# Kernel optimization log

Hardware: AMD Instinct MI355X
Metric: run time of the kernel (lower is better)

Reference implementation:

```python
import math
import jax, jax.numpy as jnp
import numpy as np

MAX_LEN = 2048
D_HEAD = 64
B, H, S = 4, 16, 1024


def setup_inputs() -> dict:
    key = jax.random.key(0)
    kq, kk, kp = jax.random.split(key, 3)
    q = jax.random.normal(kq, (B, H, S, D_HEAD), dtype=jnp.float32)
    k = jax.random.normal(kk, (B, H, S, D_HEAD), dtype=jnp.float32)
    pos_table = jax.random.normal(kp, (MAX_LEN, D_HEAD), dtype=jnp.float32)
    return {"q": q, "k": k, "pos_table": pos_table}


def reference(q, k, pos_table):
    d_head = q.shape[-1]
    seq_len = q.shape[2]
    max_len = pos_table.shape[0]
    scale = 1.0 / math.sqrt(d_head)
    # attention gates: (b,h,s,s)
    gates = jax.nn.sigmoid(jnp.einsum('bhsd,bhtd->bhst', q, k) * scale)
    # context positions: weighted sum of key indices -> (b,h,s)
    positions = jnp.arange(seq_len, dtype=q.dtype)
    ctx_pos = jnp.einsum('bhst,t->bhs', gates, positions)
    ctx_pos = jnp.clip(ctx_pos, 0.0, float(max_len - 2))
    pos_floor = ctx_pos.astype(jnp.int32)  # (b,h,s)
    pos_frac = (ctx_pos - pos_floor.astype(q.dtype))[..., None]  # (b,h,s,1)
    emb_floor = pos_table[pos_floor]  # (b,h,s,d)
    emb_ceil = pos_table[jnp.minimum(pos_floor + 1, max_len - 1)]
    pos_emb = emb_floor + pos_frac * (emb_ceil - emb_floor)  # (b,h,s,d)
    # bias: (b,h,s,s)
    bias = jnp.einsum('bhsd,bhtd->bhst', q, pos_emb)
    return bias
```

## Files before the change

### kernel.cpp

```cpp
#include <hip/hip_runtime.h>

#define Bb_ 4
#define Hh_ 16
#define Ss_ 1024
#define DH 64
#define MAXLEN 2048
#define BH (Bb_*Hh_)
#define LDST 72

typedef __attribute__((ext_vector_type(8))) short short8;
typedef __attribute__((ext_vector_type(4))) float floatx4;
typedef __attribute__((ext_vector_type(4))) unsigned short ushort4v;

static __device__ __forceinline__ unsigned short f2bf(float f) {
    unsigned int u = __builtin_bit_cast(unsigned int, f);
    u = (u + 0x7fffu + ((u >> 16) & 1u)) >> 16;
    return (unsigned short)u;
}

static __device__ __forceinline__ void stage_tile(unsigned short* lds,
                                                  const float* __restrict__ g,
                                                  int tid) {
#pragma unroll
    for (int it = 0; it < 8; ++it) {
        int idx = it * 1024 + tid * 4;
        int row = idx >> 6, col = idx & 63;
        const float4 v = *reinterpret_cast<const float4*>(g + row * 64 + col);
        ushort4v o = { f2bf(v.x), f2bf(v.y), f2bf(v.z), f2bf(v.w) };
        *reinterpret_cast<ushort4v*>(lds + row * LDST + col) = o;
    }
}

__global__ __launch_bounds__(256, 2)
void ctx_kernel(const float* __restrict__ q, const float* __restrict__ k,
                float* __restrict__ ctx) {
    __shared__ __align__(16) unsigned short Ab[128 * LDST];
    __shared__ __align__(16) unsigned short Kb[128 * LDST];

    int bx = blockIdx.x;
    int bh = bx >> 3, mt = bx & 7;
    int m0 = mt << 7;
    int tid = threadIdx.x;
    int lane = tid & 63, w = tid >> 6;
    int lo = lane & 15, quad = lane >> 4;

    stage_tile(Ab, q + (size_t)(bh * Ss_ + m0) * DH, tid);
    __syncthreads();

    short8 afr[2][2];
#pragma unroll
    for (int i = 0; i < 2; ++i)
#pragma unroll
        for (int k2 = 0; k2 < 2; ++k2)
            afr[i][k2] = *reinterpret_cast<const short8*>(
                &Ab[(w * 32 + i * 16 + lo) * LDST + k2 * 32 + quad * 8]);

    float rp[2][4];
#pragma unroll
    for (int i = 0; i < 2; ++i)
#pragma unroll
        for (int r = 0; r < 4; ++r) rp[i][r] = 0.f;

    for (int tt = 0; tt < 8; ++tt) {
        int t0 = tt << 7;
        __syncthreads();
        stage_tile(Kb, k + (size_t)(bh * Ss_ + t0) * DH, tid);
        __syncthreads();

#pragma unroll
        for (int j = 0; j < 8; ++j) {
            short8 b0 = *reinterpret_cast<const short8*>(
                &Kb[(j * 16 + lo) * LDST + 0 + quad * 8]);
            short8 b1 = *reinterpret_cast<const short8*>(
                &Kb[(j * 16 + lo) * LDST + 32 + quad * 8]);
            float tcol = (float)(t0 + j * 16 + lo);
#pragma unroll
            for (int i = 0; i < 2; ++i) {
                floatx4 c = {0.f, 0.f, 0.f, 0.f};
                c = __builtin_amdgcn_mfma_f32_16x16x32_bf16(afr[i][0], b0, c, 0, 0, 0);
                c = __builtin_amdgcn_mfma_f32_16x16x32_bf16(afr[i][1], b1, c, 0, 0, 0);
#pragma unroll
                for (int r = 0; r < 4; ++r) {
                    float x = c[r] * 0.125f;
                    float e = __expf(-x);
                    float g = __builtin_amdgcn_rcpf(1.0f + e);
                    rp[i][r] += g * tcol;
                }
            }
        }
    }

#pragma unroll
    for (int i = 0; i < 2; ++i)
#pragma unroll
        for (int r = 0; r < 4; ++r) {
            float v = rp[i][r];
            v += __shfl_xor(v, 1);
            v += __shfl_xor(v, 2);
            v += __shfl_xor(v, 4);
            v += __shfl_xor(v, 8);
            rp[i][r] = v;
        }

    if (lo == 0) {
#pragma unroll
        for (int i = 0; i < 2; ++i)
#pragma unroll
            for (int r = 0; r < 4; ++r) {
                int row = m0 + w * 32 + i * 16 + quad * 4 + r;
                float v = fminf(fmaxf(rp[i][r], 0.f), (float)(MAXLEN - 2));
                ctx[bh * Ss_ + row] = v;
            }
    }
}

__global__ __launch_bounds__(256, 2)
void bias_kernel(const float* __restrict__ q, const float* __restrict__ tb,
                 const float* __restrict__ ctx, float* __restrict__ out) {
    __shared__ __align__(16) unsigned short Ab[128 * LDST];
    __shared__ __align__(16) unsigned short Pb[128 * LDST];

    int bx = blockIdx.x;
    int bh = bx >> 6;
    int mt = (bx >> 3) & 7;
    int nt = bx & 7;
    int m0 = mt << 7, n0 = nt << 7;
    int tid = threadIdx.x;
    int lane = tid & 63, w = tid >> 6;
    int lo = lane & 15, quad = lane >> 4;

    stage_tile(Ab, q + (size_t)(bh * Ss_ + m0) * DH, tid);

    {
        int rsub = tid >> 4;
        int d0 = (tid & 15) * 4;
#pragma unroll
        for (int pass = 0; pass < 8; ++pass) {
            int row = pass * 16 + rsub;
            float c = ctx[bh * Ss_ + n0 + row];
            int fl = (int)c;
            float fr = c - (float)fl;
            int ce = min(fl + 1, MAXLEN - 1);
            const float4 e0 = *reinterpret_cast<const float4*>(tb + fl * DH + d0);
            const float4 e1 = *reinterpret_cast<const float4*>(tb + ce * DH + d0);
            ushort4v o = { f2bf(e0.x + fr * (e1.x - e0.x)),
                           f2bf(e0.y + fr * (e1.y - e0.y)),
                           f2bf(e0.z + fr * (e1.z - e0.z)),
                           f2bf(e0.w + fr * (e1.w - e0.w)) };
            *reinterpret_cast<ushort4v*>(&Pb[row * LDST + d0]) = o;
        }
    }
    __syncthreads();

    short8 afr[2][2];
#pragma unroll
    for (int i = 0; i < 2; ++i)
#pragma unroll
        for (int k2 = 0; k2 < 2; ++k2)
            afr[i][k2] = *reinterpret_cast<const short8*>(
                &Ab[(w * 32 + i * 16 + lo) * LDST + k2 * 32 + quad * 8]);

    floatx4 acc[2][8];
#pragma unroll
    for (int i = 0; i < 2; ++i)
#pragma unroll
        for (int j = 0; j < 8; ++j) acc[i][j] = (floatx4){0.f, 0.f, 0.f, 0.f};

#pragma unroll
    for (int j = 0; j < 8; ++j) {
        short8 b0 = *reinterpret_cast<const short8*>(
            &Pb[(j * 16 + lo) * LDST + 0 + quad * 8]);
        short8 b1 = *reinterpret_cast<const short8*>(
            &Pb[(j * 16 + lo) * LDST + 32 + quad * 8]);
#pragma unroll
        for (int i = 0; i < 2; ++i) {
            acc[i][j] = __builtin_amdgcn_mfma_f32_16x16x32_bf16(afr[i][0], b0, acc[i][j], 0, 0, 0);
            acc[i][j] = __builtin_amdgcn_mfma_f32_16x16x32_bf16(afr[i][1], b1, acc[i][j], 0, 0, 0);
        }
    }

#pragma unroll
    for (int i = 0; i < 2; ++i)
#pragma unroll
        for (int j = 0; j < 8; ++j)
#pragma unroll
            for (int r = 0; r < 4; ++r) {
                int row = w * 32 + i * 16 + quad * 4 + r;
                int col = j * 16 + lo;
                out[(size_t)(bh * Ss_ + m0 + row) * Ss_ + n0 + col] = acc[i][j][r];
            }
}

extern "C" void kernel_launch(void* const* d_in, const int* in_sizes, int n_in,
                              void* d_out, int out_size, void* d_ws, size_t ws_size,
                              hipStream_t stream) {
    const float* q  = (const float*)d_in[0];
    const float* k  = (const float*)d_in[1];
    const float* tb = (const float*)d_in[2];
    float* ctx = (float*)d_ws;
    float* out = (float*)d_out;

    ctx_kernel<<<BH * 8, 256, 0, stream>>>(q, k, ctx);
    bias_kernel<<<BH * 64, 256, 0, stream>>>(q, tb, ctx, out);
}
```

Before: 326.3 us.

## Fuse embedding interpolation into ctx kernel and loop bias over column tiles

The ctx kernel now interpolates the positional embeddings itself and writes them as bf16 to workspace, so the bias kernel no longer gathers from the table and redoes the interpolation for each of the 8 M tiles. The bias kernel drops to 512 blocks, each staging its q tile once and looping over 8 column tiles. It reads the B operand straight from global memory instead of LDS and writes output with nontemporal stores. The cost is 8x fewer blocks in the bias kernel, which may lower latency hiding on a store-bound 256MB output write.

```diff
diff --git a/kernel.cpp b/kernel.cpp
--- a/kernel.cpp
+++ b/kernel.cpp
@@ -32,10 +32,12 @@
 }
 
 __global__ __launch_bounds__(256, 2)
-void ctx_kernel(const float* __restrict__ q, const float* __restrict__ k,
-                float* __restrict__ ctx) {
+void ctx_emb_kernel(const float* __restrict__ q, const float* __restrict__ k,
+                    const float* __restrict__ tb,
+                    unsigned short* __restrict__ pemb) {
     __shared__ __align__(16) unsigned short Ab[128 * LDST];
     __shared__ __align__(16) unsigned short Kb[128 * LDST];
+    __shared__ float sh_ctx[128];
 
     int bx = blockIdx.x;
     int bh = bx >> 3, mt = bx & 7;
@@ -107,29 +109,11 @@
         for (int i = 0; i < 2; ++i)
 #pragma unroll
             for (int r = 0; r < 4; ++r) {
-                int row = m0 + w * 32 + i * 16 + quad * 4 + r;
-                float v = fminf(fmaxf(rp[i][r], 0.f), (float)(MAXLEN - 2));
-                ctx[bh * Ss_ + row] = v;
+                int row = w * 32 + i * 16 + quad * 4 + r;
+                sh_ctx[row] = fminf(fmaxf(rp[i][r], 0.f), (float)(MAXLEN - 2));
             }
     }
-}
-
-__global__ __launch_bounds__(256, 2)
-void bias_kernel(const float* __restrict__ q, const float* __restrict__ tb,
-                 const float* __restrict__ ctx, float* __restrict__ out) {
-    __shared__ __align__(16) unsigned short Ab[128 * LDST];
-    __shared__ __align__(16) unsigned short Pb[128 * LDST];
-
-    int bx = blockIdx.x;
-    int bh = bx >> 6;
-    int mt = (bx >> 3) & 7;
-    int nt = bx & 7;
-    int m0 = mt << 7, n0 = nt << 7;
-    int tid = threadIdx.x;
-    int lane = tid & 63, w = tid >> 6;
-    int lo = lane & 15, quad = lane >> 4;
-
-    stage_tile(Ab, q + (size_t)(bh * Ss_ + m0) * DH, tid);
+    __syncthreads();
 
     {
         int rsub = tid >> 4;
@@ -137,7 +121,7 @@
 #pragma unroll
         for (int pass = 0; pass < 8; ++pass) {
             int row = pass * 16 + rsub;
-            float c = ctx[bh * Ss_ + n0 + row];
+            float c = sh_ctx[row];
             int fl = (int)c;
             float fr = c - (float)fl;
             int ce = min(fl + 1, MAXLEN - 1);
@@ -147,9 +131,26 @@
                            f2bf(e0.y + fr * (e1.y - e0.y)),
                            f2bf(e0.z + fr * (e1.z - e0.z)),
                            f2bf(e0.w + fr * (e1.w - e0.w)) };
-            *reinterpret_cast<ushort4v*>(&Pb[row * LDST + d0]) = o;
-        }
-    }
+            *reinterpret_cast<ushort4v*>(
+                pemb + (size_t)(bh * Ss_ + m0 + row) * DH + d0) = o;
+        }
+    }
+}
+
+__global__ __launch_bounds__(256, 2)
+void bias_kernel(const float* __restrict__ q,
+                 const unsigned short* __restrict__ pemb,
+                 float* __restrict__ out) {
+    __shared__ __align__(16) unsigned short Ab[128 * LDST];
+
+    int bx = blockIdx.x;
+    int bh = bx >> 3, mt = bx & 7;
+    int m0 = mt << 7;
+    int tid = threadIdx.x;
+    int lane = tid & 63, w = tid >> 6;
+    int lo = lane & 15, quad = lane >> 4;
+
+    stage_tile(Ab, q + (size_t)(bh * Ss_ + m0) * DH, tid);
     __syncthreads();
 
     short8 afr[2][2];
@@ -160,35 +161,43 @@
             afr[i][k2] = *reinterpret_cast<const short8*>(
                 &Ab[(w * 32 + i * 16 + lo) * LDST + k2 * 32 + quad * 8]);
 
-    floatx4 acc[2][8];
-#pragma unroll
-    for (int i = 0; i < 2; ++i)
-#pragma unroll
-        for (int j = 0; j < 8; ++j) acc[i][j] = (floatx4){0.f, 0.f, 0.f, 0.f};
-
-#pragma unroll
-    for (int j = 0; j < 8; ++j) {
-        short8 b0 = *reinterpret_cast<const short8*>(
-            &Pb[(j * 16 + lo) * LDST + 0 + quad * 8]);
-        short8 b1 = *reinterpret_cast<const short8*>(
-            &Pb[(j * 16 + lo) * LDST + 32 + quad * 8]);
-#pragma unroll
-        for (int i = 0; i < 2; ++i) {
-            acc[i][j] = __builtin_amdgcn_mfma_f32_16x16x32_bf16(afr[i][0], b0, acc[i][j], 0, 0, 0);
-            acc[i][j] = __builtin_amdgcn_mfma_f32_16x16x32_bf16(afr[i][1], b1, acc[i][j], 0, 0, 0);
-        }
-    }
-
-#pragma unroll
-    for (int i = 0; i < 2; ++i)
-#pragma unroll
-        for (int j = 0; j < 8; ++j)
-#pragma unroll
-            for (int r = 0; r < 4; ++r) {
-                int row = w * 32 + i * 16 + quad * 4 + r;
-                int col = j * 16 + lo;
-                out[(size_t)(bh * Ss_ + m0 + row) * Ss_ + n0 + col] = acc[i][j][r];
+    const unsigned short* pb = pemb + (size_t)bh * Ss_ * DH;
+    float* outb = out + (size_t)(bh * Ss_ + m0) * Ss_;
+
+#pragma unroll 1
+    for (int nt = 0; nt < 8; ++nt) {
+        int n0 = nt << 7;
+
+        floatx4 acc[2][8];
+#pragma unroll
+        for (int i = 0; i < 2; ++i)
+#pragma unroll
+            for (int j = 0; j < 8; ++j) acc[i][j] = (floatx4){0.f, 0.f, 0.f, 0.f};
+
+#pragma unroll
+        for (int j = 0; j < 8; ++j) {
+            const unsigned short* bp = pb + (n0 + j * 16 + lo) * DH + quad * 8;
+            short8 b0 = *reinterpret_cast<const short8*>(bp);
+            short8 b1 = *reinterpret_cast<const short8*>(bp + 32);
+#pragma unroll
+            for (int i = 0; i < 2; ++i) {
+                acc[i][j] = __builtin_amdgcn_mfma_f32_16x16x32_bf16(afr[i][0], b0, acc[i][j], 0, 0, 0);
+                acc[i][j] = __builtin_amdgcn_mfma_f32_16x16x32_bf16(afr[i][1], b1, acc[i][j], 0, 0, 0);
             }
+        }
+
+#pragma unroll
+        for (int i = 0; i < 2; ++i)
+#pragma unroll
+            for (int j = 0; j < 8; ++j)
+#pragma unroll
+                for (int r = 0; r < 4; ++r) {
+                    int row = w * 32 + i * 16 + quad * 4 + r;
+                    int col = n0 + j * 16 + lo;
+                    __builtin_nontemporal_store(
+                        acc[i][j][r], outb + (size_t)row * Ss_ + col);
+                }
+    }
 }
 
 extern "C" void kernel_launch(void* const* d_in, const int* in_sizes, int n_in,
@@ -197,9 +206,9 @@
     const float* q  = (const float*)d_in[0];
     const float* k  = (const float*)d_in[1];
     const float* tb = (const float*)d_in[2];
-    float* ctx = (float*)d_ws;
+    unsigned short* pemb = (unsigned short*)d_ws;
     float* out = (float*)d_out;
 
-    ctx_kernel<<<BH * 8, 256, 0, stream>>>(q, k, ctx);
-    bias_kernel<<<BH * 64, 256, 0, stream>>>(q, tb, ctx, out);
-}
+    ctx_emb_kernel<<<BH * 8, 256, 0, stream>>>(q, k, tb, pemb);
+    bias_kernel<<<BH * 8, 256, 0, stream>>>(q, pemb, out);
+}
```

Result: slower. 354.5 us (+8.6%).
